# Optimization experiments

Hardware: AMD Instinct MI355X
Metric: run time of the kernel (lower is better)

## Reference

```python
import jax, jax.numpy as jnp
import numpy as np

NUM_CLASSES = 80
TOPK = 10            # matcher_hpy['topk_candicate']
ALPHA = 0.25         # focal_loss_alpha
GAMMA = 2.0          # focal_loss_gamma
REG_COST_W = 3.0     # SimOTA iou-cost weight
INVALID_COST = 1e9

B, SIDE, STRIDE, G = 16, 160, 8, 32
M = SIDE * SIDE
IMG = SIDE * STRIDE


def _bce_logits(x, t):
    # stable binary_cross_entropy_with_logits
    return t * jax.nn.softplus(-x) + (1.0 - t) * jax.nn.softplus(x)


def _box_iou_pairwise(b1, b2, eps=1e-8):
    # b1: [G,4], b2: [M,4] (xyxy) -> [G,M]
    tl = jnp.maximum(b1[:, None, :2], b2[None, :, :2])
    br = jnp.minimum(b1[:, None, 2:], b2[None, :, 2:])
    wh = jnp.clip(br - tl, 0.0)
    inter = wh[..., 0] * wh[..., 1]
    a1 = (b1[:, 2] - b1[:, 0]) * (b1[:, 3] - b1[:, 1])
    a2 = (b2[:, 2] - b2[:, 0]) * (b2[:, 3] - b2[:, 1])
    union = a1[:, None] + a2[None, :] - inter
    return inter / jnp.maximum(union, eps)


def _giou(b1, b2, eps=1e-7):
    # elementwise GIoU, b1/b2: [N,4] xyxy -> [N]
    tl = jnp.maximum(b1[..., :2], b2[..., :2])
    br = jnp.minimum(b1[..., 2:], b2[..., 2:])
    wh = jnp.clip(br - tl, 0.0)
    inter = wh[..., 0] * wh[..., 1]
    a1 = jnp.clip(b1[..., 2] - b1[..., 0], 0.0) * jnp.clip(b1[..., 3] - b1[..., 1], 0.0)
    a2 = jnp.clip(b2[..., 2] - b2[..., 0], 0.0) * jnp.clip(b2[..., 3] - b2[..., 1], 0.0)
    union = a1 + a2 - inter
    iou = inter / jnp.maximum(union, eps)
    ctl = jnp.minimum(b1[..., :2], b2[..., :2])
    cbr = jnp.maximum(b1[..., 2:], b2[..., 2:])
    cwh = jnp.clip(cbr - ctl, 0.0)
    carea = jnp.maximum(cwh[..., 0] * cwh[..., 1], eps)
    return iou - (carea - union) / carea


def _simota(anchors, pred_cls, pred_box, gt_labels, gt_boxes):
    # per-image AlignedSimOTA (mmyolo DSL-style dynamic-k assignment)
    # anchors [M,2], pred_cls [M,C] (logits, detached), pred_box [M,4], gt_labels [G], gt_boxes [G,4]
    num_gt = gt_boxes.shape[0]
    num_anchor = anchors.shape[0]
    # anchor point strictly inside gt box: [G, M]
    deltas = jnp.concatenate([anchors[None, :, :] - gt_boxes[:, None, :2],
                              gt_boxes[:, None, 2:] - anchors[None, :, :]], axis=-1)
    is_in_gt = deltas.min(axis=-1) > 0.0
    valid_anchor = is_in_gt.any(axis=0)                      # [M]
    ious = _box_iou_pairwise(gt_boxes, pred_box)             # [G, M]
    reg_cost = -jnp.log(ious + 1e-8)
    # aligned classification cost: logit at gt class, soft target = IoU
    logits = pred_cls[:, gt_labels].T                        # [G, M]
    scale = jnp.abs(ious - jax.nn.sigmoid(logits)) ** 2.0
    cls_cost = _bce_logits(logits, ious) * scale
    cost = cls_cost + REG_COST_W * reg_cost                  # [G, M]
    cost = jnp.where(valid_anchor[None, :], cost, INVALID_COST)
    # dynamic k: sum of topk ious per gt, int, clamped min 1 (<= TOPK)
    topk_ious = jax.lax.top_k(ious, TOPK)[0]                 # [G, TOPK]
    dyn_k = jnp.clip(topk_ious.sum(axis=-1).astype(jnp.int32), 1, None)  # [G]
    # lowest-cost TOPK candidates per gt, keep rank < dyn_k
    _, cand_idx = jax.lax.top_k(-cost, TOPK)                 # [G, TOPK]
    sel = (jnp.arange(TOPK)[None, :] < dyn_k[:, None]).astype(jnp.float32)
    matching = jnp.zeros((num_gt, num_anchor), jnp.float32).at[
        jnp.arange(num_gt)[:, None], cand_idx].add(sel)      # [G, M]
    fg = matching.sum(axis=0) > 0                            # [M]
    # conflicts (anchor matched to >1 gt) resolved by min cost
    matched_gt = jnp.argmin(jnp.where(matching > 0, cost, jnp.inf), axis=0)  # [M]
    labels = jnp.where(fg, gt_labels[matched_gt], NUM_CLASSES)
    boxes = jnp.where(fg[:, None], gt_boxes[matched_gt], 0.0)
    return labels, boxes


def _rand_boxes(key, shape):
    k1, k2 = jax.random.split(key)
    ctr = jax.random.uniform(k1, shape + (2,), minval=0.0, maxval=float(IMG))
    wh = jax.random.uniform(k2, shape + (2,), minval=16.0, maxval=256.0)
    return jnp.clip(jnp.concatenate([ctr - wh * 0.5, ctr + wh * 0.5], axis=-1), 0.0, float(IMG))


def setup_inputs() -> dict:
    key = jax.random.key(0)
    k0, k1, k2, k3 = jax.random.split(key, 4)
    pred_cls = jax.random.normal(k0, (B, M, NUM_CLASSES), jnp.float32) - 4.0  # background-biased logits
    pred_box = _rand_boxes(k1, (B, M))
    gt_boxes = _rand_boxes(k2, (B, G))
    gt_labels = jax.random.randint(k3, (B, G), 0, NUM_CLASSES, dtype=jnp.int32)
    ys, xs = jnp.meshgrid(jnp.arange(SIDE), jnp.arange(SIDE), indexing='ij')
    anchors = (jnp.stack([xs, ys], axis=-1).reshape(-1, 2).astype(jnp.float32) + 0.5) * STRIDE
    mask = jnp.zeros((B, M), dtype=bool)  # outputs['mask']: True = padded position
    return {"pred_cls": pred_cls, "pred_box": pred_box, "anchors": anchors,
            "gt_boxes": gt_boxes, "gt_labels": gt_labels, "mask": mask}


def reference(pred_cls, pred_box, anchors, gt_boxes, gt_labels, mask):
    C = pred_cls.shape[-1]
    # matcher consumes detached predictions
    lbl, btgt = jax.vmap(_simota, in_axes=(None, 0, 0, 0, 0))(
        anchors,
        jax.lax.stop_gradient(pred_cls),
        jax.lax.stop_gradient(pred_box),
        gt_labels, gt_boxes)
    cls_t = lbl.reshape(-1)                                   # [B*M]
    pos = cls_t != C                                          # (cls_t >= 0) always holds
    num_fgs = jnp.maximum(pos.sum().astype(jnp.float32), 1.0)
    valid = jnp.logical_not(mask.reshape(-1))                 # mask & (cls_t >= 0)
    # sigmoid focal loss over all valid anchors, one-hot targets (class C -> all-zero row)
    x = pred_cls.reshape(-1, C)
    t = jax.nn.one_hot(cls_t, C, dtype=x.dtype)
    p = jax.nn.sigmoid(x)
    ce = _bce_logits(x, t)
    p_t = p * t + (1.0 - p) * (1.0 - t)
    focal = ce * (1.0 - p_t) ** GAMMA * (ALPHA * t + (1.0 - ALPHA) * (1.0 - t))
    loss_cls = (focal * valid[:, None].astype(x.dtype)).sum() / num_fgs
    # GIoU loss over positives
    g = _giou(pred_box.reshape(-1, 4), btgt.reshape(-1, 4))
    loss_giou = ((1.0 - g) * pos.astype(x.dtype)).sum() / num_fgs
    return jnp.stack([loss_cls, loss_giou])
```

## Files before the change

### kernel.cpp

```cpp
#include <hip/hip_runtime.h>
#include <cstdint>
#include <cstddef>

#define NB 16
#define SIDE 160
#define MM (SIDE*SIDE)
#define NC 80
#define NG 32
#define TOPK 10
#define REGW 3.0f
#define INVC 1e9f

using ull = unsigned long long;

__device__ __forceinline__ unsigned f2sort(float f) {
    unsigned b = __float_as_uint(f);
    return b ^ ((unsigned)((int)b >> 31) | 0x80000000u);
}
__device__ __forceinline__ float rcpf(float x) { return __builtin_amdgcn_rcpf(x); }

__device__ __forceinline__ float f_bg(float x) {
    float e  = __expf(-fabsf(x));
    float rc = rcpf(1.f + e);
    float p  = (x >= 0.f) ? rc : e*rc;
    float sp = fmaxf(x, 0.f) + __logf(1.f + e);
    return sp*p*p*0.75f;
}
__device__ __forceinline__ float f_fg(float x) {
    float e  = __expf(-fabsf(x));
    float rc = rcpf(1.f + e);
    float p  = (x >= 0.f) ? rc : e*rc;
    float sp = fmaxf(x, 0.f) + __logf(1.f + e);
    float om = 1.f - p;
    return (sp - x)*om*om*0.25f;
}

__global__ __launch_bounds__(256) void k_valid(const float* __restrict__ anchors,
                                               const float* __restrict__ gt_boxes,
                                               unsigned char* __restrict__ valid) {
    int i = blockIdx.x * 256 + threadIdx.x;
    int b = i / MM, m = i % MM;
    float ax = anchors[2*m], ay = anchors[2*m+1];
    const float* gb = gt_boxes + b*NG*4;
    unsigned char v = 0;
    for (int g = 0; g < NG; ++g) {
        float x1 = gb[4*g], y1 = gb[4*g+1], x2 = gb[4*g+2], y2 = gb[4*g+3];
        float d = fminf(fminf(ax-x1, ay-y1), fminf(x2-ax, y2-ay));
        v |= (d > 0.f) ? 1 : 0;
    }
    valid[i] = v;
}

__global__ __launch_bounds__(512, 8) void k_cost(
    const float* __restrict__ pred_cls, const float* __restrict__ pred_box,
    const float* __restrict__ gt_boxes, const int* __restrict__ gt_labels,
    const unsigned char* __restrict__ valid, const unsigned char* __restrict__ mask,
    unsigned* __restrict__ cost_part, unsigned* __restrict__ iou_part,
    float* __restrict__ accum, int nchunk)
{
    __shared__ float s_gtb[128];
    __shared__ int s_lab[32];
    __shared__ float s_red[8];

    int blk = blockIdx.x;
    int b = blk / nchunk, chunk = blk - b*nchunk;
    int A = MM / nchunk;
    int nsub = A >> 6;
    int tid = threadIdx.x;
    int g = tid >> 4, j = tid & 15;

    if (tid < 128) s_gtb[tid] = gt_boxes[b*NG*4 + tid];
    if (tid < 32)  s_lab[tid] = gt_labels[b*NG + tid];
    __syncthreads();

    float gx1 = s_gtb[g*4+0], gy1 = s_gtb[g*4+1];
    float gx2 = s_gtb[g*4+2], gy2 = s_gtb[g*4+3];
    int   lab = s_lab[g];
    float garea = (gx2-gx1)*(gy2-gy1);

    unsigned lc[TOPK], li[TOPK];
    #pragma unroll
    for (int t = 0; t < TOPK; ++t) { lc[t] = 0xFFFFFFFFu; li[t] = 0xFFFFFFFFu; }
    float bgsum = 0.f;

    int m0 = chunk * A;
    for (int s = 0; s < nsub; ++s) {
        int mbase = m0 + s*64;
        size_t gbase = (size_t)b*MM + mbase;
        const float4* gcls = (const float4*)(pred_cls + gbase*NC);
        #pragma unroll
        for (int q = 0; q < 3; ++q) {
            int idx = tid + 512*q;
            if (idx < 1280) {
                float4 v = gcls[idx];
                int a = idx / 20;
                if (!mask[gbase + a])
                    bgsum += f_bg(v.x) + f_bg(v.y) + f_bg(v.z) + f_bg(v.w);
            }
        }
        #pragma unroll
        for (int k = 0; k < 4; ++k) {
            int a = j + 16*k;
            unsigned m = (unsigned)(mbase + a);
            size_t gi = gbase + a;
            float4 pb = ((const float4*)pred_box)[gi];
            float l  = pred_cls[gi*NC + lab];
            unsigned char vld = valid[gi];
            float iw = fmaxf(fminf(gx2, pb.z) - fmaxf(gx1, pb.x), 0.f);
            float ih = fmaxf(fminf(gy2, pb.w) - fmaxf(gy1, pb.y), 0.f);
            float inter = iw*ih;
            float pa = (pb.z-pb.x)*(pb.w-pb.y);
            float uni = garea + pa - inter;
            float iou = inter * rcpf(fmaxf(uni, 1e-8f));
            float e  = __expf(-fabsf(l));
            float rc = rcpf(1.f + e);
            float sg = (l >= 0.f) ? rc : e*rc;
            float sp_pos = fmaxf(l, 0.f) + __logf(1.f + e);
            float sp_neg = sp_pos - l;
            float bce = iou*sp_neg + (1.f-iou)*sp_pos;
            float dd = iou - sg;
            float cost = bce*dd*dd - REGW*__logf(iou + 1e-8f);
            if (!vld) cost = INVC;
            unsigned cur = (f2sort(cost) & 0xFFFF8000u) | m;
            #pragma unroll
            for (int t = 0; t < TOPK; ++t) {
                unsigned mn = min(lc[t], cur), mx = max(lc[t], cur);
                lc[t] = mn; cur = mx;
            }
            cur = (~f2sort(iou) & 0xFFFF8000u) | m;
            #pragma unroll
            for (int t = 0; t < TOPK; ++t) {
                unsigned mn = min(li[t], cur), mx = max(li[t], cur);
                li[t] = mn; cur = mx;
            }
        }
    }
    size_t pbase = ((size_t)(b*NG + g)*nchunk + chunk)*TOPK;
    #pragma unroll
    for (int r = 0; r < TOPK; ++r) {
        unsigned h = lc[0];
        h = min(h, (unsigned)__shfl_xor((int)h, 1));
        h = min(h, (unsigned)__shfl_xor((int)h, 2));
        h = min(h, (unsigned)__shfl_xor((int)h, 4));
        h = min(h, (unsigned)__shfl_xor((int)h, 8));
        if (lc[0] == h) {
            #pragma unroll
            for (int t = 0; t < TOPK-1; ++t) lc[t] = lc[t+1];
            lc[TOPK-1] = 0xFFFFFFFFu;
        }
        if (j == 0) cost_part[pbase + r] = h;
    }
    #pragma unroll
    for (int r = 0; r < TOPK; ++r) {
        unsigned h = li[0];
        h = min(h, (unsigned)__shfl_xor((int)h, 1));
        h = min(h, (unsigned)__shfl_xor((int)h, 2));
        h = min(h, (unsigned)__shfl_xor((int)h, 4));
        h = min(h, (unsigned)__shfl_xor((int)h, 8));
        if (li[0] == h) {
            #pragma unroll
            for (int t = 0; t < TOPK-1; ++t) li[t] = li[t+1];
            li[TOPK-1] = 0xFFFFFFFFu;
        }
        if (j == 0) iou_part[pbase + r] = h;
    }
    for (int o = 32; o; o >>= 1) bgsum += __shfl_down(bgsum, o);
    int ln = tid & 63, wv = tid >> 6;
    if (ln == 0) s_red[wv] = bgsum;
    __syncthreads();
    if (tid == 0) {
        float sum = 0.f;
        #pragma unroll
        for (int w = 0; w < 8; ++w) sum += s_red[w];
        atomicAdd(&accum[0], sum);
    }
}

__global__ __launch_bounds__(256) void k_merge(
    const unsigned* __restrict__ cost_part, const unsigned* __restrict__ iou_part,
    const float* __restrict__ pred_cls, const float* __restrict__ pred_box,
    const float* __restrict__ gt_boxes, const int* __restrict__ gt_labels,
    const unsigned char* __restrict__ valid,
    ull* __restrict__ best, int nchunk)
{
    int lane = threadIdx.x & 63, wv = threadIdx.x >> 6;
    int bg = blockIdx.x*4 + wv;
    int b = bg >> 5, g = bg & (NG-1);
    int nent = nchunk * TOPK;
    size_t base = (size_t)bg * nent;

    float gx1 = gt_boxes[bg*4+0], gy1 = gt_boxes[bg*4+1];
    float gx2 = gt_boxes[bg*4+2], gy2 = gt_boxes[bg*4+3];
    int   lab = gt_labels[bg];
    float garea = (gx2-gx1)*(gy2-gy1);

    unsigned l10[TOPK];
    #pragma unroll
    for (int t = 0; t < TOPK; ++t) l10[t] = 0xFFFFFFFFu;
    for (int q = 0; q*64 < nent; ++q) {
        int e = lane + 64*q;
        unsigned cur = (e < nent) ? iou_part[base + e] : 0xFFFFFFFFu;
        #pragma unroll
        for (int t = 0; t < TOPK; ++t) {
            unsigned mn = min(l10[t], cur), mx = max(l10[t], cur);
            l10[t] = mn; cur = mx;
        }
    }
    unsigned ioukey = 0xFFFFFFFFu;
    #pragma unroll
    for (int r = 0; r < TOPK; ++r) {
        unsigned h = l10[0];
        #pragma unroll
        for (int mlt = 1; mlt < 64; mlt <<= 1)
            h = min(h, (unsigned)__shfl_xor((int)h, mlt));
        if (l10[0] == h) {
            #pragma unroll
            for (int t = 0; t < TOPK-1; ++t) l10[t] = l10[t+1];
            l10[TOPK-1] = 0xFFFFFFFFu;
        }
        if (lane == r) ioukey = h;
    }
    float myiou = 0.f;
    if (lane < TOPK) {
        int m = (int)(ioukey & 0x7FFFu);
        float4 pb = ((const float4*)pred_box)[(size_t)b*MM + m];
        float iw = fmaxf(fminf(gx2, pb.z) - fmaxf(gx1, pb.x), 0.f);
        float ih = fmaxf(fminf(gy2, pb.w) - fmaxf(gy1, pb.y), 0.f);
        float inter = iw*ih;
        float pa = (pb.z-pb.x)*(pb.w-pb.y);
        float uni = garea + pa - inter;
        myiou = inter / fmaxf(uni, 1e-8f);
    }
    #pragma unroll
    for (int mlt = 1; mlt < 64; mlt <<= 1) myiou += __shfl_xor(myiou, mlt);
    int dynk = (int)myiou; if (dynk < 1) dynk = 1;

    #pragma unroll
    for (int t = 0; t < TOPK; ++t) l10[t] = 0xFFFFFFFFu;
    for (int q = 0; q*64 < nent; ++q) {
        int e = lane + 64*q;
        unsigned cur = (e < nent) ? cost_part[base + e] : 0xFFFFFFFFu;
        #pragma unroll
        for (int t = 0; t < TOPK; ++t) {
            unsigned mn = min(l10[t], cur), mx = max(l10[t], cur);
            l10[t] = mn; cur = mx;
        }
    }
    unsigned costkey = 0xFFFFFFFFu;
    #pragma unroll
    for (int r = 0; r < TOPK; ++r) {
        unsigned h = l10[0];
        #pragma unroll
        for (int mlt = 1; mlt < 64; mlt <<= 1)
            h = min(h, (unsigned)__shfl_xor((int)h, mlt));
        if (l10[0] == h) {
            #pragma unroll
            for (int t = 0; t < TOPK-1; ++t) l10[t] = l10[t+1];
            l10[TOPK-1] = 0xFFFFFFFFu;
        }
        if (lane == r) costkey = h;
    }
    if (lane < dynk) {
        unsigned m = costkey & 0x7FFFu;
        size_t gi = (size_t)b*MM + m;
        float cost;
        if (!valid[gi]) {
            cost = INVC;
        } else {
            float4 pb = ((const float4*)pred_box)[gi];
            float iw = fmaxf(fminf(gx2, pb.z) - fmaxf(gx1, pb.x), 0.f);
            float ih = fmaxf(fminf(gy2, pb.w) - fmaxf(gy1, pb.y), 0.f);
            float inter = iw*ih;
            float pa = (pb.z-pb.x)*(pb.w-pb.y);
            float uni = garea + pa - inter;
            float iou = inter / fmaxf(uni, 1e-8f);
            float l = pred_cls[gi*NC + lab];
            float e  = expf(-fabsf(l));
            float p  = 1.f/(1.f + e);
            float sg = (l >= 0.f) ? p : e*p;
            float sp_pos = fmaxf(l, 0.f) + log1pf(e);
            float sp_neg = sp_pos - l;
            float bce = iou*sp_neg + (1.f-iou)*sp_pos;
            float dd = iou - sg;
            cost = bce*dd*dd - REGW*logf(iou + 1e-8f);
        }
        atomicMin(&best[(size_t)b*MM + m], ((ull)f2sort(cost) << 32) | (unsigned)g);
    }
}

__global__ __launch_bounds__(256) void k_post(
    const float* __restrict__ pred_cls, const float* __restrict__ pred_box,
    const float* __restrict__ gt_boxes, const int* __restrict__ gt_labels,
    const unsigned char* __restrict__ mask, const ull* __restrict__ best,
    float* __restrict__ accum)
{
    int i = blockIdx.x*256 + threadIdx.x;
    int b = i / MM;
    ull key = best[i];
    float cls_c = 0.f, giou_c = 0.f, cnt = 0.f;
    if (key != ~0ull) {
        int g = (int)(key & 0xFFFFFFFFull);
        int bgi = b*NG + g;
        float4 pb = *(const float4*)(pred_box + (size_t)i*4);
        float gx1 = gt_boxes[bgi*4],   gy1 = gt_boxes[bgi*4+1];
        float gx2 = gt_boxes[bgi*4+2], gy2 = gt_boxes[bgi*4+3];
        float iw = fmaxf(fminf(pb.z,gx2) - fmaxf(pb.x,gx1), 0.f);
        float ih = fmaxf(fminf(pb.w,gy2) - fmaxf(pb.y,gy1), 0.f);
        float inter = iw*ih;
        float a1 = fmaxf(pb.z-pb.x,0.f)*fmaxf(pb.w-pb.y,0.f);
        float a2 = fmaxf(gx2-gx1,0.f)*fmaxf(gy2-gy1,0.f);
        float uni = a1 + a2 - inter;
        float iou = inter / fmaxf(uni, 1e-7f);
        float cw = fmaxf(fmaxf(pb.z,gx2) - fminf(pb.x,gx1), 0.f);
        float ch = fmaxf(fmaxf(pb.w,gy2) - fminf(pb.y,gy1), 0.f);
        float ca = fmaxf(cw*ch, 1e-7f);
        float giou = iou - (ca - uni)/ca;
        giou_c = 1.f - giou;
        cnt = 1.f;
        if (!mask[i]) {
            int lab = gt_labels[bgi];
            float x = pred_cls[(size_t)i*NC + lab];
            cls_c = f_fg(x) - f_bg(x);
        }
    }
    for (int o = 32; o; o >>= 1) {
        cls_c  += __shfl_down(cls_c, o);
        giou_c += __shfl_down(giou_c, o);
        cnt    += __shfl_down(cnt, o);
    }
    __shared__ float sc[4], sg_[4], sn[4];
    int ln = threadIdx.x & 63, wv = threadIdx.x >> 6;
    if (ln == 0) { sc[wv] = cls_c; sg_[wv] = giou_c; sn[wv] = cnt; }
    __syncthreads();
    if (threadIdx.x == 0) {
        atomicAdd(&accum[0], sc[0]+sc[1]+sc[2]+sc[3]);
        float gtot = sg_[0]+sg_[1]+sg_[2]+sg_[3];
        float ntot = sn[0]+sn[1]+sn[2]+sn[3];
        if (gtot != 0.f || ntot != 0.f) {
            atomicAdd(&accum[1], gtot);
            atomicAdd(&accum[2], ntot);
        }
    }
}

__global__ void k_final(const float* __restrict__ accum, float* __restrict__ out) {
    if (threadIdx.x == 0) {
        float nf = fmaxf(accum[2], 1.f);
        out[0] = accum[0]/nf;
        out[1] = accum[1]/nf;
    }
}

extern "C" void kernel_launch(void* const* d_in, const int* in_sizes, int n_in,
                              void* d_out, int out_size, void* d_ws, size_t ws_size,
                              hipStream_t stream) {
    const float* pred_cls  = (const float*)d_in[0];
    const float* pred_box  = (const float*)d_in[1];
    const float* anchors   = (const float*)d_in[2];
    const float* gt_boxes  = (const float*)d_in[3];
    const int*   gt_labels = (const int*)d_in[4];
    const unsigned char* mask = (const unsigned char*)d_in[5];
    float* out = (float*)d_out;

    auto need = [](int nc) -> size_t {
        return 256 + (size_t)NB*MM*8 + (size_t)NB*MM + 2*(size_t)NB*NG*nc*TOPK*4;
    };
    int nchunk = 80;
    if (ws_size < need(80)) nchunk = 40;
    if (ws_size < need(40)) nchunk = 25;
    if (ws_size < need(25)) return;

    char* ws = (char*)d_ws;
    float* accum = (float*)ws;
    ull* best = (ull*)(ws + 256);
    unsigned char* valid = (unsigned char*)(ws + 256 + (size_t)NB*MM*8);
    unsigned* cost_part = (unsigned*)(ws + 256 + (size_t)NB*MM*8 + (size_t)NB*MM);
    unsigned* iou_part  = cost_part + (size_t)NB*NG*nchunk*TOPK;

    hipMemsetAsync(accum, 0, 16, stream);
    hipMemsetAsync(best, 0xFF, (size_t)NB*MM*8, stream);

    k_valid<<<NB*MM/256, 256, 0, stream>>>(anchors, gt_boxes, valid);
    k_cost <<<NB*nchunk, 512, 0, stream>>>(pred_cls, pred_box, gt_boxes, gt_labels,
                                           valid, mask, cost_part, iou_part, accum, nchunk);
    k_merge<<<NB*NG/4,   256, 0, stream>>>(cost_part, iou_part, pred_cls, pred_box,
                                           gt_boxes, gt_labels, valid, best, nchunk);
    k_post <<<NB*MM/256, 256, 0, stream>>>(pred_cls, pred_box, gt_boxes, gt_labels,
                                           mask, best, accum);
    k_final<<<1, 64, 0, stream>>>(accum, out);
}
```

Before: 169.1 us.

## Split background focal sum into own kernel and skip invalid-anchor cost work

Moves the background focal-loss reduction over all class logits out of the cost kernel into a dedicated grid-stride kernel. The cost kernel then computes cost only for anchors inside some GT box and inserts INVALID keys only when an image has fewer than TOPK valid anchors, using a per-image valid count gathered with a ballot in the validity kernel. Top-k insertion sequences are skipped with an early compare against the current worst entry, both in the cost kernel and in the merge kernel. This adds a kernel launch and another full read of pred_cls in a separate pass. It also adds branch divergence in the inner loop.

```diff
diff --git a/kernel.cpp b/kernel.cpp
--- a/kernel.cpp
+++ b/kernel.cpp
@@ -37,7 +37,8 @@
 
 __global__ __launch_bounds__(256) void k_valid(const float* __restrict__ anchors,
                                                const float* __restrict__ gt_boxes,
-                                               unsigned char* __restrict__ valid) {
+                                               unsigned char* __restrict__ valid,
+                                               int* __restrict__ vcount) {
     int i = blockIdx.x * 256 + threadIdx.x;
     int b = i / MM, m = i % MM;
     float ax = anchors[2*m], ay = anchors[2*m+1];
@@ -49,23 +50,43 @@
         v |= (d > 0.f) ? 1 : 0;
     }
     valid[i] = v;
-}
-
-__global__ __launch_bounds__(512, 8) void k_cost(
+    ull bal = __ballot(v != 0);
+    if ((threadIdx.x & 63) == 0 && bal)
+        atomicAdd(&vcount[b], (int)__popcll(bal));
+}
+
+__global__ __launch_bounds__(256) void k_bg(const float* __restrict__ pred_cls,
+                                            const unsigned char* __restrict__ mask,
+                                            float* __restrict__ accum) {
+    const unsigned total4 = (unsigned)NB*MM*NC/4;
+    unsigned stride = gridDim.x * blockDim.x;
+    float acc = 0.f;
+    for (unsigned i4 = blockIdx.x*blockDim.x + threadIdx.x; i4 < total4; i4 += stride) {
+        float4 v = ((const float4*)pred_cls)[i4];
+        unsigned row = i4 / 20;
+        if (!mask[row])
+            acc += f_bg(v.x) + f_bg(v.y) + f_bg(v.z) + f_bg(v.w);
+    }
+    for (int o = 32; o; o >>= 1) acc += __shfl_down(acc, o);
+    __shared__ float sw[4];
+    int ln = threadIdx.x & 63, wv = threadIdx.x >> 6;
+    if (ln == 0) sw[wv] = acc;
+    __syncthreads();
+    if (threadIdx.x == 0) atomicAdd(&accum[0], sw[0]+sw[1]+sw[2]+sw[3]);
+}
+
+__global__ __launch_bounds__(512, 4) void k_cost(
     const float* __restrict__ pred_cls, const float* __restrict__ pred_box,
     const float* __restrict__ gt_boxes, const int* __restrict__ gt_labels,
-    const unsigned char* __restrict__ valid, const unsigned char* __restrict__ mask,
-    unsigned* __restrict__ cost_part, unsigned* __restrict__ iou_part,
-    float* __restrict__ accum, int nchunk)
+    const unsigned char* __restrict__ valid, const int* __restrict__ vcount,
+    unsigned* __restrict__ cost_part, unsigned* __restrict__ iou_part, int nchunk)
 {
     __shared__ float s_gtb[128];
     __shared__ int s_lab[32];
-    __shared__ float s_red[8];
 
     int blk = blockIdx.x;
     int b = blk / nchunk, chunk = blk - b*nchunk;
     int A = MM / nchunk;
-    int nsub = A >> 6;
     int tid = threadIdx.x;
     int g = tid >> 4, j = tid & 15;
 
@@ -77,41 +98,37 @@
     float gx2 = s_gtb[g*4+2], gy2 = s_gtb[g*4+3];
     int   lab = s_lab[g];
     float garea = (gx2-gx1)*(gy2-gy1);
+    bool rare = (vcount[b] < TOPK);
+    unsigned invckey = f2sort(INVC) & 0xFFFF8000u;
+
+    const float4* pbb = (const float4*)pred_box + (size_t)b*MM;
+    const float*  pcb = pred_cls + (size_t)b*MM*NC;
+    const unsigned char* vb = valid + (size_t)b*MM;
 
     unsigned lc[TOPK], li[TOPK];
     #pragma unroll
     for (int t = 0; t < TOPK; ++t) { lc[t] = 0xFFFFFFFFu; li[t] = 0xFFFFFFFFu; }
-    float bgsum = 0.f;
 
     int m0 = chunk * A;
-    for (int s = 0; s < nsub; ++s) {
-        int mbase = m0 + s*64;
-        size_t gbase = (size_t)b*MM + mbase;
-        const float4* gcls = (const float4*)(pred_cls + gbase*NC);
-        #pragma unroll
-        for (int q = 0; q < 3; ++q) {
-            int idx = tid + 512*q;
-            if (idx < 1280) {
-                float4 v = gcls[idx];
-                int a = idx / 20;
-                if (!mask[gbase + a])
-                    bgsum += f_bg(v.x) + f_bg(v.y) + f_bg(v.z) + f_bg(v.w);
+    for (int a0 = 0; a0 < A; a0 += 16) {
+        int m = m0 + a0 + j;
+        float4 pb = pbb[m];
+        float iw = fmaxf(fminf(gx2, pb.z) - fmaxf(gx1, pb.x), 0.f);
+        float ih = fmaxf(fminf(gy2, pb.w) - fmaxf(gy1, pb.y), 0.f);
+        float inter = iw*ih;
+        float pa = (pb.z-pb.x)*(pb.w-pb.y);
+        float uni = garea + pa - inter;
+        float iou = inter * rcpf(fmaxf(uni, 1e-8f));
+        unsigned cur = (~f2sort(iou) & 0xFFFF8000u) | (unsigned)m;
+        if (cur < li[TOPK-1]) {
+            #pragma unroll
+            for (int t = 0; t < TOPK; ++t) {
+                unsigned mn = min(li[t], cur), mx = max(li[t], cur);
+                li[t] = mn; cur = mx;
             }
         }
-        #pragma unroll
-        for (int k = 0; k < 4; ++k) {
-            int a = j + 16*k;
-            unsigned m = (unsigned)(mbase + a);
-            size_t gi = gbase + a;
-            float4 pb = ((const float4*)pred_box)[gi];
-            float l  = pred_cls[gi*NC + lab];
-            unsigned char vld = valid[gi];
-            float iw = fmaxf(fminf(gx2, pb.z) - fmaxf(gx1, pb.x), 0.f);
-            float ih = fmaxf(fminf(gy2, pb.w) - fmaxf(gy1, pb.y), 0.f);
-            float inter = iw*ih;
-            float pa = (pb.z-pb.x)*(pb.w-pb.y);
-            float uni = garea + pa - inter;
-            float iou = inter * rcpf(fmaxf(uni, 1e-8f));
+        if (vb[m]) {
+            float l = pcb[m*NC + lab];
             float e  = __expf(-fabsf(l));
             float rc = rcpf(1.f + e);
             float sg = (l >= 0.f) ? rc : e*rc;
@@ -120,18 +137,22 @@
             float bce = iou*sp_neg + (1.f-iou)*sp_pos;
             float dd = iou - sg;
             float cost = bce*dd*dd - REGW*__logf(iou + 1e-8f);
-            if (!vld) cost = INVC;
-            unsigned cur = (f2sort(cost) & 0xFFFF8000u) | m;
-            #pragma unroll
-            for (int t = 0; t < TOPK; ++t) {
-                unsigned mn = min(lc[t], cur), mx = max(lc[t], cur);
-                lc[t] = mn; cur = mx;
+            unsigned ck = (f2sort(cost) & 0xFFFF8000u) | (unsigned)m;
+            if (ck < lc[TOPK-1]) {
+                #pragma unroll
+                for (int t = 0; t < TOPK; ++t) {
+                    unsigned mn = min(lc[t], ck), mx = max(lc[t], ck);
+                    lc[t] = mn; ck = mx;
+                }
             }
-            cur = (~f2sort(iou) & 0xFFFF8000u) | m;
-            #pragma unroll
-            for (int t = 0; t < TOPK; ++t) {
-                unsigned mn = min(li[t], cur), mx = max(li[t], cur);
-                li[t] = mn; cur = mx;
+        } else if (rare) {
+            unsigned ck = invckey | (unsigned)m;
+            if (ck < lc[TOPK-1]) {
+                #pragma unroll
+                for (int t = 0; t < TOPK; ++t) {
+                    unsigned mn = min(lc[t], ck), mx = max(lc[t], ck);
+                    lc[t] = mn; ck = mx;
+                }
             }
         }
     }
@@ -163,16 +184,6 @@
             li[TOPK-1] = 0xFFFFFFFFu;
         }
         if (j == 0) iou_part[pbase + r] = h;
-    }
-    for (int o = 32; o; o >>= 1) bgsum += __shfl_down(bgsum, o);
-    int ln = tid & 63, wv = tid >> 6;
-    if (ln == 0) s_red[wv] = bgsum;
-    __syncthreads();
-    if (tid == 0) {
-        float sum = 0.f;
-        #pragma unroll
-        for (int w = 0; w < 8; ++w) sum += s_red[w];
-        atomicAdd(&accum[0], sum);
     }
 }
 
@@ -200,10 +211,12 @@
     for (int q = 0; q*64 < nent; ++q) {
         int e = lane + 64*q;
         unsigned cur = (e < nent) ? iou_part[base + e] : 0xFFFFFFFFu;
-        #pragma unroll
-        for (int t = 0; t < TOPK; ++t) {
-            unsigned mn = min(l10[t], cur), mx = max(l10[t], cur);
-            l10[t] = mn; cur = mx;
+        if (cur < l10[TOPK-1]) {
+            #pragma unroll
+            for (int t = 0; t < TOPK; ++t) {
+                unsigned mn = min(l10[t], cur), mx = max(l10[t], cur);
+                l10[t] = mn; cur = mx;
+            }
         }
     }
     unsigned ioukey = 0xFFFFFFFFu;
@@ -240,10 +253,12 @@
     for (int q = 0; q*64 < nent; ++q) {
         int e = lane + 64*q;
         unsigned cur = (e < nent) ? cost_part[base + e] : 0xFFFFFFFFu;
-        #pragma unroll
-        for (int t = 0; t < TOPK; ++t) {
-            unsigned mn = min(l10[t], cur), mx = max(l10[t], cur);
-            l10[t] = mn; cur = mx;
+        if (cur < l10[TOPK-1]) {
+            #pragma unroll
+            for (int t = 0; t < TOPK; ++t) {
+                unsigned mn = min(l10[t], cur), mx = max(l10[t], cur);
+                l10[t] = mn; cur = mx;
+            }
         }
     }
     unsigned costkey = 0xFFFFFFFFu;
@@ -372,17 +387,19 @@
 
     char* ws = (char*)d_ws;
     float* accum = (float*)ws;
+    int* vcount  = (int*)(ws + 64);
     ull* best = (ull*)(ws + 256);
     unsigned char* valid = (unsigned char*)(ws + 256 + (size_t)NB*MM*8);
     unsigned* cost_part = (unsigned*)(ws + 256 + (size_t)NB*MM*8 + (size_t)NB*MM);
     unsigned* iou_part  = cost_part + (size_t)NB*NG*nchunk*TOPK;
 
-    hipMemsetAsync(accum, 0, 16, stream);
+    hipMemsetAsync(accum, 0, 256, stream);
     hipMemsetAsync(best, 0xFF, (size_t)NB*MM*8, stream);
 
-    k_valid<<<NB*MM/256, 256, 0, stream>>>(anchors, gt_boxes, valid);
+    k_valid<<<NB*MM/256, 256, 0, stream>>>(anchors, gt_boxes, valid, vcount);
+    k_bg   <<<2048, 256, 0, stream>>>(pred_cls, mask, accum);
     k_cost <<<NB*nchunk, 512, 0, stream>>>(pred_cls, pred_box, gt_boxes, gt_labels,
-                                           valid, mask, cost_part, iou_part, accum, nchunk);
+                                           valid, vcount, cost_part, iou_part, nchunk);
     k_merge<<<NB*NG/4,   256, 0, stream>>>(cost_part, iou_part, pred_cls, pred_box,
                                            gt_boxes, gt_labels, valid, best, nchunk);
     k_post <<<NB*MM/256, 256, 0, stream>>>(pred_cls, pred_box, gt_boxes, gt_labels,
```

New measurement: 237.9 us. 1.41x slower.
